# Optimization experiments

Hardware: AMD Instinct MI355X
Metric: run time of the kernel (lower is better)

## Reference

```python
import jax, jax.numpy as jnp
import numpy as np

N = 100000
E = 3200000
F_IN = 128
HID = 16
C = 8


def setup_inputs() -> dict:
    key = jax.random.key(0)
    k1, k2, k3, k4 = jax.random.split(key, 4)
    x = jax.random.normal(k1, (N, F_IN), dtype=jnp.float32)
    edge_index = jax.random.randint(k2, (2, E), 0, N, dtype=jnp.int64)
    W1 = jax.random.normal(k3, (F_IN, HID), dtype=jnp.float32) * (1.0 / np.sqrt(F_IN))
    b1 = jnp.zeros((HID,), dtype=jnp.float32)
    W2 = jax.random.normal(k4, (HID, C), dtype=jnp.float32) * (1.0 / np.sqrt(HID))
    b2 = jnp.zeros((C,), dtype=jnp.float32)
    return {"x": x, "edge_index": edge_index, "W1": W1, "b1": b1, "W2": W2, "b2": b2, "num_nodes": N}


def gcn_conv(x, src, dst, norm, W, b, num_nodes):
    # x: [N, F_in], src/dst: [E+N] (self-loops appended), norm: [E+N]
    h = x @ W                                # dense transform first (small out dim)
    msg = h[src] * norm[:, None]             # gather + edgewise scale
    out = jax.ops.segment_sum(msg, dst, num_segments=num_nodes)  # scatter-add
    return out + b


def reference(x, edge_index, W1, b1, W2, b2, num_nodes):
    # GCN normalization with self-loops: D^-1/2 (A+I) D^-1/2
    loop = jnp.arange(num_nodes, dtype=edge_index.dtype)
    src = jnp.concatenate([edge_index[0], loop])
    dst = jnp.concatenate([edge_index[1], loop])
    deg = jax.ops.segment_sum(jnp.ones_like(dst, dtype=x.dtype), dst, num_segments=num_nodes)
    dinv = jnp.where(deg > 0, jax.lax.rsqrt(deg), 0.0)
    norm = dinv[src] * dinv[dst]             # [E+N]

    h = jax.nn.relu(gcn_conv(x, src, dst, norm, W1, b1, num_nodes))
    # Dropout(p=0.5) in eval mode -> identity
    logits = gcn_conv(h, src, dst, norm, W2, b2, num_nodes)
    return jax.nn.log_softmax(logits, axis=1)
```

## Files before the change

### kernel.cpp

```cpp
#include <hip/hip_runtime.h>
#include <hip/hip_fp16.h>
#include <math.h>

#define FIN 128
#define HID 16
#define NC 8
#define BSH 8
#define BUKN 256
#define MAXBUK 512
#define CAP 10240
#define EPT 8
#define ACH (512 * EPT)

__global__ void setup_kernel(const void* __restrict__ ei, int E, int N,
                             int* __restrict__ flag, int* __restrict__ pcur,
                             int nbuk) {
    int b = blockIdx.x * blockDim.x + threadIdx.x;
    if (b < nbuk) pcur[b * 16] = b * CAP;
    if (b == 0) {
        const long long* p = (const long long*)ei;
        int ok = 1;
        for (int i = 0; i < 16; ++i) {
            long long v = p[i];
            if (v < 0 || v >= (long long)N) { ok = 0; break; }
        }
        *flag = ok;
    }
}

__global__ __launch_bounds__(512) void passA_kernel(
        const void* __restrict__ ei, int E, const int* __restrict__ flag,
        int* __restrict__ pcur, unsigned* __restrict__ pakbuf, int nbuk) {
    const int is64 = *flag;
    const int* __restrict__ e32 = (const int*)ei;
    const int vecOK = is64 ? ((E & 1) == 0) : ((E & 3) == 0);
    __shared__ int cnt[MAXBUK], scn[MAXBUK], sbase[MAXBUK];
    __shared__ unsigned spv[ACH];
    __shared__ unsigned short sbk[ACH];
    const int t = threadIdx.x;
    for (long long c0 = (long long)blockIdx.x * ACH; c0 < E;
         c0 += (long long)gridDim.x * ACH) {
        cnt[t] = 0;
        __syncthreads();
        const long long e0 = c0 + (long long)t * EPT;
        const bool full = vecOK && (e0 + EPT <= E);
        int bv[EPT], rk[EPT];
        unsigned pv[EPT];
        if (full) {
            int ds[EPT], ss[EPT];
            if (is64) {
                const int4* pd = (const int4*)(e32 + 2 * ((long long)E + e0));
                const int4* ps = (const int4*)(e32 + 2 * e0);
                int4 a = pd[0], b = pd[1], c = pd[2], d = pd[3];
                ds[0]=a.x; ds[1]=a.z; ds[2]=b.x; ds[3]=b.z;
                ds[4]=c.x; ds[5]=c.z; ds[6]=d.x; ds[7]=d.z;
                int4 e = ps[0], f = ps[1], g = ps[2], h = ps[3];
                ss[0]=e.x; ss[1]=e.z; ss[2]=f.x; ss[3]=f.z;
                ss[4]=g.x; ss[5]=g.z; ss[6]=h.x; ss[7]=h.z;
            } else {
                const int4* pd = (const int4*)(e32 + (long long)E + e0);
                const int4* ps = (const int4*)(e32 + e0);
                int4 a = pd[0], b = pd[1];
                ds[0]=a.x; ds[1]=a.y; ds[2]=a.z; ds[3]=a.w;
                ds[4]=b.x; ds[5]=b.y; ds[6]=b.z; ds[7]=b.w;
                int4 e = ps[0], f = ps[1];
                ss[0]=e.x; ss[1]=e.y; ss[2]=e.z; ss[3]=e.w;
                ss[4]=f.x; ss[5]=f.y; ss[6]=f.z; ss[7]=f.w;
            }
#pragma unroll
            for (int i = 0; i < EPT; ++i) {
                int dd = ds[i];
                bv[i] = dd >> BSH;
                pv[i] = (unsigned)ss[i] | ((unsigned)(dd & (BUKN - 1)) << 24);
                rk[i] = atomicAdd(&cnt[bv[i]], 1);
            }
        } else {
#pragma unroll
            for (int i = 0; i < EPT; ++i) {
                long long e = e0 + i;
                bv[i] = -1;
                if (e < E) {
                    int dd = e32[is64 ? 2 * ((long long)E + e) : ((long long)E + e)];
                    int ssc = e32[is64 ? 2 * e : e];
                    bv[i] = dd >> BSH;
                    pv[i] = (unsigned)ssc | ((unsigned)(dd & (BUKN - 1)) << 24);
                    rk[i] = atomicAdd(&cnt[bv[i]], 1);
                }
            }
        }
        __syncthreads();
        int v = cnt[t];
        scn[t] = v;
        __syncthreads();
        for (int d = 1; d < MAXBUK; d <<= 1) {
            int add = (t >= d) ? scn[t - d] : 0;
            __syncthreads();
            scn[t] += add;
            __syncthreads();
        }
        int excl = scn[t] - v;
        __syncthreads();
        scn[t] = excl;
        if (t < nbuk) sbase[t] = v ? atomicAdd(&pcur[t * 16], v) : 0;
        __syncthreads();
#pragma unroll
        for (int i = 0; i < EPT; ++i) {
            if (bv[i] >= 0) {
                int s = scn[bv[i]] + rk[i];
                spv[s] = pv[i];
                sbk[s] = (unsigned short)bv[i];
            }
        }
        __syncthreads();
        int total = (int)((E - c0 < ACH) ? (E - c0) : ACH);
        for (int s = t; s < total; s += 512) {
            int b = sbk[s];
            int gpos = sbase[b] + (s - scn[b]);
            if (gpos < (b + 1) * CAP) pakbuf[gpos] = spv[s];
        }
        __syncthreads();
    }
}

__global__ __launch_bounds__(512) void passC2_kernel(
        const unsigned* __restrict__ pak, const int* __restrict__ pcur,
        int* __restrict__ csr_src, int* __restrict__ off,
        float* __restrict__ dinv, int N) {
    __shared__ int c[BUKN], sc[BUKN], cur[BUKN];
    const int b = blockIdx.x, t = threadIdx.x;
    if (t < BUKN) c[t] = 0;
    __syncthreads();
    const int ebeg = b * CAP;
    int eend = pcur[b * 16];
    if (eend > ebeg + CAP) eend = ebeg + CAP;
    for (int i = ebeg + t; i < eend; i += 512)
        atomicAdd(&c[pak[i] >> 24], 1);
    __syncthreads();
    int v = (t < BUKN) ? c[t] : 0;
    if (t < BUKN) sc[t] = v;
    __syncthreads();
    for (int d = 1; d < 256; d <<= 1) {
        int add = (t < BUKN && t >= d) ? sc[t - d] : 0;
        __syncthreads();
        if (t < BUKN) sc[t] += add;
        __syncthreads();
    }
    if (t < BUKN) cur[t] = ebeg + sc[t] - v;
    __syncthreads();
    for (int i = ebeg + t; i < eend; i += 512) {
        unsigned w = pak[i];
        int pos = atomicAdd(&cur[w >> 24], 1);
        csr_src[pos] = (int)(w & 0xFFFFFFu);
    }
    __syncthreads();
    int n = (b << BSH) + t;
    if (t < BUKN && n < N) {
        off[n] = cur[t];
        dinv[n] = rsqrtf((float)(v + 1));
    }
}

__global__ void transform1_kernel(const float* __restrict__ x,
                                  const float* __restrict__ W1,
                                  const float* __restrict__ dinv,
                                  __half* __restrict__ g1, int N) {
    __shared__ float xs[16][FIN + 4];
    __shared__ float w[FIN][HID];
    const int t = threadIdx.x;
    for (int i = t; i < FIN * HID; i += 256) w[i / HID][i % HID] = W1[i];

    const float4* x4 = (const float4*)x;
    for (int rb = blockIdx.x * 16; rb < N; rb += gridDim.x * 16) {
        __syncthreads();
        for (int i = t; i < 16 * FIN / 4; i += 256) {
            int r = i >> 5, f4 = i & 31;
            int row = rb + r;
            float4 v = (row < N) ? x4[(size_t)row * (FIN / 4) + f4]
                                 : make_float4(0.f, 0.f, 0.f, 0.f);
            *((float4*)&xs[r][f4 * 4]) = v;
        }
        __syncthreads();
        int r = t >> 4, k = t & 15;
        int row = rb + r;
        if (row < N) {
            float s = 0.f;
#pragma unroll
            for (int f = 0; f < FIN; ++f) s += xs[r][f] * w[f][k];
            g1[(size_t)row * HID + k] = __float2half(s * dinv[row]);
        }
    }
}

__global__ void agg1_kernel(const int* __restrict__ off, const int* __restrict__ csr_src,
                            const __half2* __restrict__ g1h, const float* __restrict__ dinv,
                            const float* __restrict__ b1, const float* __restrict__ W2,
                            float4* __restrict__ g2q_out, int N) {
    const float4* g1q = (const float4*)g1h;
    __shared__ float w2s[HID][NC];
    for (int i = threadIdx.x; i < HID * NC; i += blockDim.x)
        w2s[i >> 3][i & 7] = W2[i];
    __syncthreads();
    int wid = threadIdx.x >> 6;
    int lane = threadIdx.x & 63;
    int sub = lane >> 4;
    int r = lane & 15;
    int hi = r & 1;
    int j = r >> 1;
    float4 bA = ((const float4*)b1)[hi * 2];
    float4 bB = ((const float4*)b1)[hi * 2 + 1];
    int wavesTotal = gridDim.x * (blockDim.x >> 6);
    for (int base = (blockIdx.x * (blockDim.x >> 6) + wid) * 4; base < N;
         base += wavesTotal * 4) {
        int n = base + sub;
        bool act = n < N;
        int start = 0, end = 0;
        float4 selfraw;
        if (act) {
            start = (n & (BUKN - 1)) ? off[n - 1] : (n >> BSH) * CAP;
            end = off[n];
            if (r < 2) selfraw = g1q[(size_t)n * 2 + hi];
        }
        float s0=0.f,s1=0.f,s2=0.f,s3=0.f,s4=0.f,s5=0.f,s6=0.f,s7=0.f;
        for (int e = start + j; e < end; e += 8) {
            float4 raw = g1q[(size_t)csr_src[e] * 2 + hi];
            float2 f0 = __half22float2(*(__half2*)&raw.x);
            float2 f1 = __half22float2(*(__half2*)&raw.y);
            float2 f2 = __half22float2(*(__half2*)&raw.z);
            float2 f3 = __half22float2(*(__half2*)&raw.w);
            s0 += f0.x; s1 += f0.y; s2 += f1.x; s3 += f1.y;
            s4 += f2.x; s5 += f2.y; s6 += f3.x; s7 += f3.y;
        }
#pragma unroll
        for (int m = 2; m <= 8; m <<= 1) {
            s0 += __shfl_xor(s0, m, 64); s1 += __shfl_xor(s1, m, 64);
            s2 += __shfl_xor(s2, m, 64); s3 += __shfl_xor(s3, m, 64);
            s4 += __shfl_xor(s4, m, 64); s5 += __shfl_xor(s5, m, 64);
            s6 += __shfl_xor(s6, m, 64); s7 += __shfl_xor(s7, m, 64);
        }
        if (act && r < 2) {
            float di = dinv[n];
            float2 f0 = __half22float2(*(__half2*)&selfraw.x);
            float2 f1 = __half22float2(*(__half2*)&selfraw.y);
            float2 f2 = __half22float2(*(__half2*)&selfraw.z);
            float2 f3 = __half22float2(*(__half2*)&selfraw.w);
            float h8[8];
            h8[0] = fmaxf(di * (s0 + f0.x) + bA.x, 0.f);
            h8[1] = fmaxf(di * (s1 + f0.y) + bA.y, 0.f);
            h8[2] = fmaxf(di * (s2 + f1.x) + bA.z, 0.f);
            h8[3] = fmaxf(di * (s3 + f1.y) + bA.w, 0.f);
            h8[4] = fmaxf(di * (s4 + f2.x) + bB.x, 0.f);
            h8[5] = fmaxf(di * (s5 + f2.y) + bB.y, 0.f);
            h8[6] = fmaxf(di * (s6 + f3.x) + bB.z, 0.f);
            h8[7] = fmaxf(di * (s7 + f3.y) + bB.w, 0.f);
            float part[8];
#pragma unroll
            for (int c = 0; c < 8; ++c) {
                float acc = 0.f;
#pragma unroll
                for (int k = 0; k < 8; ++k) acc += h8[k] * w2s[hi * 8 + k][c];
                part[c] = acc;
            }
#pragma unroll
            for (int c = 0; c < 8; ++c) part[c] += __shfl_xor(part[c], 1, 64);
            if (r == 0) {
                __half2 p0 = __floats2half2_rn(part[0] * di, part[1] * di);
                __half2 p1 = __floats2half2_rn(part[2] * di, part[3] * di);
                __half2 p2 = __floats2half2_rn(part[4] * di, part[5] * di);
                __half2 p3 = __floats2half2_rn(part[6] * di, part[7] * di);
                float4 o;
                *(__half2*)&o.x = p0; *(__half2*)&o.y = p1;
                *(__half2*)&o.z = p2; *(__half2*)&o.w = p3;
                g2q_out[n] = o;
            }
        }
    }
}

__global__ void agg2_kernel(const int* __restrict__ off, const int* __restrict__ csr_src,
                            const __half2* __restrict__ g2h, const float* __restrict__ dinv,
                            const float* __restrict__ b2, float* __restrict__ out, int N) {
    const float4* g2q = (const float4*)g2h;
    int wid = threadIdx.x >> 6;
    int lane = threadIdx.x & 63;
    int sub = lane >> 3, sl = lane & 7;
    float4 b2A = ((const float4*)b2)[0];
    float4 b2B = ((const float4*)b2)[1];
    int wavesTotal = gridDim.x * (blockDim.x >> 6);
    for (int base = (blockIdx.x * (blockDim.x >> 6) + wid) * 8; base < N;
         base += wavesTotal * 8) {
        int n = base + sub;
        bool act = n < N;
        int start = 0, end = 0;
        float4 selfraw;
        if (act) {
            start = (n & (BUKN - 1)) ? off[n - 1] : (n >> BSH) * CAP;
            end = off[n];
            selfraw = g2q[n];
        }
        float s0=0.f,s1=0.f,s2=0.f,s3=0.f,s4=0.f,s5=0.f,s6=0.f,s7=0.f;
        for (int e = start + sl; e < end; e += 8) {
            float4 raw = g2q[csr_src[e]];
            float2 f0 = __half22float2(*(__half2*)&raw.x);
            float2 f1 = __half22float2(*(__half2*)&raw.y);
            float2 f2 = __half22float2(*(__half2*)&raw.z);
            float2 f3 = __half22float2(*(__half2*)&raw.w);
            s0 += f0.x; s1 += f0.y; s2 += f1.x; s3 += f1.y;
            s4 += f2.x; s5 += f2.y; s6 += f3.x; s7 += f3.y;
        }
#pragma unroll
        for (int m = 1; m <= 4; m <<= 1) {
            s0 += __shfl_xor(s0, m, 64); s1 += __shfl_xor(s1, m, 64);
            s2 += __shfl_xor(s2, m, 64); s3 += __shfl_xor(s3, m, 64);
            s4 += __shfl_xor(s4, m, 64); s5 += __shfl_xor(s5, m, 64);
            s6 += __shfl_xor(s6, m, 64); s7 += __shfl_xor(s7, m, 64);
        }
        if (act) {
            float di = dinv[n];
            float2 f0 = __half22float2(*(__half2*)&selfraw.x);
            float2 f1 = __half22float2(*(__half2*)&selfraw.y);
            float2 f2 = __half22float2(*(__half2*)&selfraw.z);
            float2 f3 = __half22float2(*(__half2*)&selfraw.w);
            float l0 = di * (s0 + f0.x) + b2A.x;
            float l1 = di * (s1 + f0.y) + b2A.y;
            float l2 = di * (s2 + f1.x) + b2A.z;
            float l3 = di * (s3 + f1.y) + b2A.w;
            float l4 = di * (s4 + f2.x) + b2B.x;
            float l5 = di * (s5 + f2.y) + b2B.y;
            float l6 = di * (s6 + f3.x) + b2B.z;
            float l7 = di * (s7 + f3.y) + b2B.w;
            float m0 = fmaxf(fmaxf(fmaxf(l0, l1), fmaxf(l2, l3)),
                             fmaxf(fmaxf(l4, l5), fmaxf(l6, l7)));
            float se = __expf(l0 - m0) + __expf(l1 - m0) + __expf(l2 - m0) +
                       __expf(l3 - m0) + __expf(l4 - m0) + __expf(l5 - m0) +
                       __expf(l6 - m0) + __expf(l7 - m0);
            float lse = m0 + __logf(se);
            if (sl < 2) {
                float4 o;
                if (sl == 0) { o.x=l0-lse; o.y=l1-lse; o.z=l2-lse; o.w=l3-lse; }
                else         { o.x=l4-lse; o.y=l5-lse; o.z=l6-lse; o.w=l7-lse; }
                ((float4*)&out[(size_t)n * NC])[sl] = o;
            }
        }
    }
}

extern "C" void kernel_launch(void* const* d_in, const int* in_sizes, int n_in,
                              void* d_out, int out_size, void* d_ws, size_t ws_size,
                              hipStream_t stream) {
    const float* x  = (const float*)d_in[0];
    const void*  ei = d_in[1];
    const float* W1 = (const float*)d_in[2];
    const float* b1 = (const float*)d_in[3];
    const float* W2 = (const float*)d_in[4];
    const float* b2 = (const float*)d_in[5];

    const int N = in_sizes[0] / FIN;
    const int E = in_sizes[1] / 2;
    const int nbuk = (N + BUKN - 1) >> BSH;

    char* p = (char*)d_ws;
    unsigned* pakbuf = (unsigned*)p;     p += (size_t)nbuk * CAP * 4;
    int*    csr_src = (int*)p;           p += (size_t)nbuk * CAP * 4;
    __half* g1h     = (__half*)p;        p += (size_t)N * HID * 2;
    __half* g2h     = (__half*)p;        p += (size_t)N * NC * 2;
    int*    off     = (int*)p;           p += (size_t)N * 4;
    float*  dinv    = (float*)p;         p += (size_t)N * 4;
    int*    pcur    = (int*)p;           p += (size_t)MAXBUK * 16 * 4;
    int*    flag    = (int*)p;

    setup_kernel<<<(nbuk + 255) / 256, 256, 0, stream>>>(ei, E, N, flag, pcur, nbuk);
    passA_kernel<<<(E + ACH - 1) / ACH, 512, 0, stream>>>(ei, E, flag, pcur,
                                                          pakbuf, nbuk);
    passC2_kernel<<<nbuk, 512, 0, stream>>>(pakbuf, pcur, csr_src, off, dinv, N);

    transform1_kernel<<<(N + 15) / 16, 256, 0, stream>>>(x, W1, dinv, g1h, N);
    agg1_kernel<<<(N + 15) / 16, 256, 0, stream>>>(off, csr_src, (const __half2*)g1h,
                                                   dinv, b1, W2, (float4*)g2h, N);
    agg2_kernel<<<(N + 31) / 32, 256, 0, stream>>>(off, csr_src, (const __half2*)g2h,
                                                   dinv, b2, (float*)d_out, N);
}
```

Measured before the change: 137.7 us.

## Accumulate aggregation in packed fp16, fold setup into passA, cap transform grid

The neighbor-sum loops in both aggregation kernels now accumulate in packed half2 adds instead of converting each gathered value to fp32. Shuffle reductions also run on packed halves. This cuts ALU and register work in the gather-bound loops, at the cost of fp16 rounding and overflow risk when summing many neighbors. Separately, the setup kernel is removed: the index-width check moves into every passA block, bucket cursors become relative counts zeroed by a memset, and the transform1 grid is capped at 2048 blocks.

```diff
diff --git a/kernel.cpp b/kernel.cpp
--- a/kernel.cpp
+++ b/kernel.cpp
@@ -12,26 +12,23 @@
 #define EPT 8
 #define ACH (512 * EPT)
 
-__global__ void setup_kernel(const void* __restrict__ ei, int E, int N,
-                             int* __restrict__ flag, int* __restrict__ pcur,
-                             int nbuk) {
-    int b = blockIdx.x * blockDim.x + threadIdx.x;
-    if (b < nbuk) pcur[b * 16] = b * CAP;
-    if (b == 0) {
-        const long long* p = (const long long*)ei;
-        int ok = 1;
-        for (int i = 0; i < 16; ++i) {
-            long long v = p[i];
-            if (v < 0 || v >= (long long)N) { ok = 0; break; }
-        }
-        *flag = ok;
-    }
+__device__ __forceinline__ __half2 shfl2(__half2 v, int m) {
+    unsigned u = *(unsigned*)&v;
+    u = __shfl_xor(u, m, 64);
+    return *(__half2*)&u;
 }
 
 __global__ __launch_bounds__(512) void passA_kernel(
-        const void* __restrict__ ei, int E, const int* __restrict__ flag,
+        const void* __restrict__ ei, int E, int N,
         int* __restrict__ pcur, unsigned* __restrict__ pakbuf, int nbuk) {
-    const int is64 = *flag;
+    const long long* p64 = (const long long*)ei;
+    int ok = 1;
+#pragma unroll
+    for (int i = 0; i < 16; ++i) {
+        long long v = p64[i];
+        if (v < 0 || v >= (long long)N) ok = 0;
+    }
+    const int is64 = ok;
     const int* __restrict__ e32 = (const int*)ei;
     const int vecOK = is64 ? ((E & 1) == 0) : ((E & 3) == 0);
     __shared__ int cnt[MAXBUK], scn[MAXBUK], sbase[MAXBUK];
@@ -115,8 +112,8 @@
         int total = (int)((E - c0 < ACH) ? (E - c0) : ACH);
         for (int s = t; s < total; s += 512) {
             int b = sbk[s];
-            int gpos = sbase[b] + (s - scn[b]);
-            if (gpos < (b + 1) * CAP) pakbuf[gpos] = spv[s];
+            int rel = sbase[b] + (s - scn[b]);
+            if (rel < CAP) pakbuf[b * CAP + rel] = spv[s];
         }
         __syncthreads();
     }
@@ -131,8 +128,9 @@
     if (t < BUKN) c[t] = 0;
     __syncthreads();
     const int ebeg = b * CAP;
-    int eend = pcur[b * 16];
-    if (eend > ebeg + CAP) eend = ebeg + CAP;
+    int cntb = pcur[b * 16];
+    if (cntb > CAP) cntb = CAP;
+    const int eend = ebeg + cntb;
     for (int i = ebeg + t; i < eend; i += 512)
         atomicAdd(&c[pak[i] >> 24], 1);
     __syncthreads();
@@ -220,38 +218,35 @@
             end = off[n];
             if (r < 2) selfraw = g1q[(size_t)n * 2 + hi];
         }
-        float s0=0.f,s1=0.f,s2=0.f,s3=0.f,s4=0.f,s5=0.f,s6=0.f,s7=0.f;
+        __half2 a0 = __float2half2_rn(0.f), a1 = a0, a2 = a0, a3 = a0;
         for (int e = start + j; e < end; e += 8) {
             float4 raw = g1q[(size_t)csr_src[e] * 2 + hi];
-            float2 f0 = __half22float2(*(__half2*)&raw.x);
-            float2 f1 = __half22float2(*(__half2*)&raw.y);
-            float2 f2 = __half22float2(*(__half2*)&raw.z);
-            float2 f3 = __half22float2(*(__half2*)&raw.w);
-            s0 += f0.x; s1 += f0.y; s2 += f1.x; s3 += f1.y;
-            s4 += f2.x; s5 += f2.y; s6 += f3.x; s7 += f3.y;
+            const __half2* rh = (const __half2*)&raw;
+            a0 = __hadd2(a0, rh[0]); a1 = __hadd2(a1, rh[1]);
+            a2 = __hadd2(a2, rh[2]); a3 = __hadd2(a3, rh[3]);
         }
 #pragma unroll
         for (int m = 2; m <= 8; m <<= 1) {
-            s0 += __shfl_xor(s0, m, 64); s1 += __shfl_xor(s1, m, 64);
-            s2 += __shfl_xor(s2, m, 64); s3 += __shfl_xor(s3, m, 64);
-            s4 += __shfl_xor(s4, m, 64); s5 += __shfl_xor(s5, m, 64);
-            s6 += __shfl_xor(s6, m, 64); s7 += __shfl_xor(s7, m, 64);
+            a0 = __hadd2(a0, shfl2(a0, m)); a1 = __hadd2(a1, shfl2(a1, m));
+            a2 = __hadd2(a2, shfl2(a2, m)); a3 = __hadd2(a3, shfl2(a3, m));
         }
         if (act && r < 2) {
             float di = dinv[n];
+            float2 s01 = __half22float2(a0), s23 = __half22float2(a1);
+            float2 s45 = __half22float2(a2), s67 = __half22float2(a3);
             float2 f0 = __half22float2(*(__half2*)&selfraw.x);
             float2 f1 = __half22float2(*(__half2*)&selfraw.y);
             float2 f2 = __half22float2(*(__half2*)&selfraw.z);
             float2 f3 = __half22float2(*(__half2*)&selfraw.w);
             float h8[8];
-            h8[0] = fmaxf(di * (s0 + f0.x) + bA.x, 0.f);
-            h8[1] = fmaxf(di * (s1 + f0.y) + bA.y, 0.f);
-            h8[2] = fmaxf(di * (s2 + f1.x) + bA.z, 0.f);
-            h8[3] = fmaxf(di * (s3 + f1.y) + bA.w, 0.f);
-            h8[4] = fmaxf(di * (s4 + f2.x) + bB.x, 0.f);
-            h8[5] = fmaxf(di * (s5 + f2.y) + bB.y, 0.f);
-            h8[6] = fmaxf(di * (s6 + f3.x) + bB.z, 0.f);
-            h8[7] = fmaxf(di * (s7 + f3.y) + bB.w, 0.f);
+            h8[0] = fmaxf(di * (s01.x + f0.x) + bA.x, 0.f);
+            h8[1] = fmaxf(di * (s01.y + f0.y) + bA.y, 0.f);
+            h8[2] = fmaxf(di * (s23.x + f1.x) + bA.z, 0.f);
+            h8[3] = fmaxf(di * (s23.y + f1.y) + bA.w, 0.f);
+            h8[4] = fmaxf(di * (s45.x + f2.x) + bB.x, 0.f);
+            h8[5] = fmaxf(di * (s45.y + f2.y) + bB.y, 0.f);
+            h8[6] = fmaxf(di * (s67.x + f3.x) + bB.z, 0.f);
+            h8[7] = fmaxf(di * (s67.y + f3.y) + bB.w, 0.f);
             float part[8];
 #pragma unroll
             for (int c = 0; c < 8; ++c) {
@@ -297,37 +292,34 @@
             end = off[n];
             selfraw = g2q[n];
         }
-        float s0=0.f,s1=0.f,s2=0.f,s3=0.f,s4=0.f,s5=0.f,s6=0.f,s7=0.f;
+        __half2 a0 = __float2half2_rn(0.f), a1 = a0, a2 = a0, a3 = a0;
         for (int e = start + sl; e < end; e += 8) {
             float4 raw = g2q[csr_src[e]];
-            float2 f0 = __half22float2(*(__half2*)&raw.x);
-            float2 f1 = __half22float2(*(__half2*)&raw.y);
-            float2 f2 = __half22float2(*(__half2*)&raw.z);
-            float2 f3 = __half22float2(*(__half2*)&raw.w);
-            s0 += f0.x; s1 += f0.y; s2 += f1.x; s3 += f1.y;
-            s4 += f2.x; s5 += f2.y; s6 += f3.x; s7 += f3.y;
+            const __half2* rh = (const __half2*)&raw;
+            a0 = __hadd2(a0, rh[0]); a1 = __hadd2(a1, rh[1]);
+            a2 = __hadd2(a2, rh[2]); a3 = __hadd2(a3, rh[3]);
         }
 #pragma unroll
         for (int m = 1; m <= 4; m <<= 1) {
-            s0 += __shfl_xor(s0, m, 64); s1 += __shfl_xor(s1, m, 64);
-            s2 += __shfl_xor(s2, m, 64); s3 += __shfl_xor(s3, m, 64);
-            s4 += __shfl_xor(s4, m, 64); s5 += __shfl_xor(s5, m, 64);
-            s6 += __shfl_xor(s6, m, 64); s7 += __shfl_xor(s7, m, 64);
+            a0 = __hadd2(a0, shfl2(a0, m)); a1 = __hadd2(a1, shfl2(a1, m));
+            a2 = __hadd2(a2, shfl2(a2, m)); a3 = __hadd2(a3, shfl2(a3, m));
         }
         if (act) {
             float di = dinv[n];
+            float2 s01 = __half22float2(a0), s23 = __half22float2(a1);
+            float2 s45 = __half22float2(a2), s67 = __half22float2(a3);
             float2 f0 = __half22float2(*(__half2*)&selfraw.x);
             float2 f1 = __half22float2(*(__half2*)&selfraw.y);
             float2 f2 = __half22float2(*(__half2*)&selfraw.z);
             float2 f3 = __half22float2(*(__half2*)&selfraw.w);
-            float l0 = di * (s0 + f0.x) + b2A.x;
-            float l1 = di * (s1 + f0.y) + b2A.y;
-            float l2 = di * (s2 + f1.x) + b2A.z;
-            float l3 = di * (s3 + f1.y) + b2A.w;
-            float l4 = di * (s4 + f2.x) + b2B.x;
-            float l5 = di * (s5 + f2.y) + b2B.y;
-            float l6 = di * (s6 + f3.x) + b2B.z;
-            float l7 = di * (s7 + f3.y) + b2B.w;
+            float l0 = di * (s01.x + f0.x) + b2A.x;
+            float l1 = di * (s01.y + f0.y) + b2A.y;
+            float l2 = di * (s23.x + f1.x) + b2A.z;
+            float l3 = di * (s23.y + f1.y) + b2A.w;
+            float l4 = di * (s45.x + f2.x) + b2B.x;
+            float l5 = di * (s45.y + f2.y) + b2B.y;
+            float l6 = di * (s67.x + f3.x) + b2B.z;
+            float l7 = di * (s67.y + f3.y) + b2B.w;
             float m0 = fmaxf(fmaxf(fmaxf(l0, l1), fmaxf(l2, l3)),
                              fmaxf(fmaxf(l4, l5), fmaxf(l6, l7)));
             float se = __expf(l0 - m0) + __expf(l1 - m0) + __expf(l2 - m0) +
@@ -366,14 +358,14 @@
     int*    off     = (int*)p;           p += (size_t)N * 4;
     float*  dinv    = (float*)p;         p += (size_t)N * 4;
     int*    pcur    = (int*)p;           p += (size_t)MAXBUK * 16 * 4;
-    int*    flag    = (int*)p;
-
-    setup_kernel<<<(nbuk + 255) / 256, 256, 0, stream>>>(ei, E, N, flag, pcur, nbuk);
-    passA_kernel<<<(E + ACH - 1) / ACH, 512, 0, stream>>>(ei, E, flag, pcur,
+
+    hipMemsetAsync(pcur, 0, (size_t)MAXBUK * 16 * 4, stream);
+    passA_kernel<<<(E + ACH - 1) / ACH, 512, 0, stream>>>(ei, E, N, pcur,
                                                           pakbuf, nbuk);
     passC2_kernel<<<nbuk, 512, 0, stream>>>(pakbuf, pcur, csr_src, off, dinv, N);
 
-    transform1_kernel<<<(N + 15) / 16, 256, 0, stream>>>(x, W1, dinv, g1h, N);
+    int t1grid = (N + 15) / 16; if (t1grid > 2048) t1grid = 2048;
+    transform1_kernel<<<t1grid, 256, 0, stream>>>(x, W1, dinv, g1h, N);
     agg1_kernel<<<(N + 15) / 16, 256, 0, stream>>>(off, csr_src, (const __half2*)g1h,
                                                    dinv, b1, W2, (float4*)g2h, N);
     agg2_kernel<<<(N + 31) / 32, 256, 0, stream>>>(off, csr_src, (const __half2*)g2h,
```

Measured after the change: 135.4 us. About the same (-1.6%).
